# Kernel tuning notes

Hardware: AMD Instinct MI355X
Metric: run time of the kernel (lower is better)

The kernel has to match this reference:

```python
import jax, jax.numpy as jnp
import numpy as np

NBINS = 256


def _getmask(mi):
    # mi: [h, w] image already scaled to [0, 255]
    # torch.histc(mi, bins=256, min=0, max=255): values outside [0,255] ignored
    hist = jax.lax.stop_gradient(
        jnp.histogram(mi, bins=NBINS, range=(0.0, 255.0))[0].astype(jnp.float32)
    )
    # mask_output[i] = sum_j |j - i| * hist[j]  -> small 256x256 matvec
    j = jnp.arange(NBINS, dtype=jnp.float32)
    dist = jnp.abs(j[:, None] - j[None, :])  # [256, 256]
    mask_output = dist @ hist                 # [256]
    # mask[image==i] = mask_output[i]; only exact-integer pixels in [0,255] match
    r = jnp.round(mi)
    valid = (mi == r) & (r >= 0.0) & (r <= 255.0)
    idx = jnp.clip(r, 0.0, 255.0).astype(jnp.int32)
    mask = jnp.where(valid, mask_output[idx], 0.0)
    # if mask.max()==0: return zeros; else return the (scaled) image itself
    return jnp.where(mask.max() == 0.0, jnp.zeros_like(mi), mi)


def _forward(image_irr, image_vis):
    irr = image_irr * 255.0
    _vis = image_vis * 255.0  # computed but unused in the original forward
    mi = irr[:, 0, :, :]                       # [b, h, w]
    masked = jax.vmap(_getmask)(mi) / 255.0    # [b, h, w]
    msk_ir = masked[:, None, :, :]             # [b, 1, h, w]
    msk = jnp.stack([msk_ir, 1.0 - msk_ir], axis=0)  # [2, b, 1, h, w]
    msks = jax.nn.softmax(msk, axis=0)
    return msks[0], msks[1]


def setup_inputs() -> dict:
    key = jax.random.key(0)
    k1, k2 = jax.random.split(key)
    shape = (16, 1, 1024, 1024)
    # quantized pixels so that image*255 is (mostly) exactly integer,
    # matching the module's implicit assumption (histc + equality tests)
    image_irr = jax.random.randint(k1, shape, 0, 256).astype(jnp.float32) / 255.0
    image_vis = jax.random.randint(k2, shape, 0, 256).astype(jnp.float32) / 255.0
    return {"image_irr": image_irr, "image_vis": image_vis}


def reference(image_irr, image_vis):
    return _forward(image_irr, image_vis)
```

## Files before the change

### kernel.cpp

```cpp
#include <hip/hip_runtime.h>
#include <stdint.h>

#define BATCH 16
#define HW (1024*1024)
#define NPIX (BATCH * HW)
#define SBLK 64

typedef float vf4 __attribute__((ext_vector_type(4)));

__global__ __launch_bounds__(256) void scan_kernel(const float* __restrict__ in,
                                                   uint2* __restrict__ partials) {
    const int tid = threadIdx.x;
    const int batch = blockIdx.y;
    int minb = 0x7FFF, maxb = -1, valid = 0;

    const vf4* src = (const vf4*)(in + (size_t)batch * HW) + (size_t)blockIdx.x * 4096;
    for (int i = tid; i < 4096; i += 256) {
        vf4 x = __builtin_nontemporal_load(&src[i]);
        float v[4] = {x.x, x.y, x.z, x.w};
#pragma unroll
        for (int k = 0; k < 4; ++k) {
            float mi = v[k] * 255.0f;
            if (mi >= 0.0f && mi <= 255.0f) {
                int b = (int)(mi * (256.0f / 255.0f));
                if (b > 255) b = 255;
                minb = min(minb, b);
                maxb = max(maxb, b);
                valid |= (mi == rintf(mi)) ? 1 : 0;
            }
        }
    }
#pragma unroll
    for (int off = 32; off > 0; off >>= 1) {
        minb  = min(minb, __shfl_xor(minb, off));
        maxb  = max(maxb, __shfl_xor(maxb, off));
        valid |= __shfl_xor(valid, off);
    }
    __shared__ int sm[4], sx[4], sv[4];
    const int w = tid >> 6;
    if ((tid & 63) == 0) { sm[w] = minb; sx[w] = maxb; sv[w] = valid; }
    __syncthreads();
    if (tid == 0) {
#pragma unroll
        for (int i = 1; i < 4; ++i) {
            minb  = min(minb, sm[i]);
            maxb  = max(maxb, sx[i]);
            valid |= sv[i];
        }
        uint2 p;
        p.x = ((unsigned)(minb & 0xFFFF) << 16) | (unsigned)(maxb & 0xFFFF);
        p.y = (unsigned)valid;
        partials[batch * SBLK + blockIdx.x] = p;
    }
}

__global__ __launch_bounds__(64) void flag_kernel(const uint2* __restrict__ partials,
                                                  unsigned* __restrict__ flags) {
    const int b = blockIdx.x;
    const int t = threadIdx.x;
    uint2 p = partials[b * SBLK + t];
    int minb = (int)(short)(p.x >> 16);
    int maxb = (int)(short)(p.x & 0xFFFF);
    unsigned valid = p.y;
#pragma unroll
    for (int off = 32; off > 0; off >>= 1) {
        minb = min(minb, __shfl_xor(minb, off));
        maxb = max(maxb, __shfl_xor(maxb, off));
        valid |= (unsigned)__shfl_xor((int)valid, off);
    }
    if (t == 0) flags[b] = (valid && (minb != maxb)) ? 1u : 0u;
}

__device__ __forceinline__ float2 softmax2(float x, float fm) {
    float mi = x * 255.0f;
    float m = (mi / 255.0f) * fm;
    float e = expf(1.0f - 2.0f * m);
    float r = 1.0f / (1.0f + e);
    return make_float2(r, e * r);
}

__global__ __launch_bounds__(256) void out_kernel(const float* __restrict__ in,
                                                  const unsigned* __restrict__ flags,
                                                  float* __restrict__ out) {
    const int batch = blockIdx.x >> 10;
    const float fm = flags[batch] ? 1.0f : 0.0f;
    const size_t i4 = (size_t)blockIdx.x * 256 + threadIdx.x;
    vf4 x = __builtin_nontemporal_load(&((const vf4*)in)[i4]);
    float2 rx = softmax2(x.x, fm);
    float2 ry = softmax2(x.y, fm);
    float2 rz = softmax2(x.z, fm);
    float2 rw = softmax2(x.w, fm);
    vf4 o0 = {rx.x, ry.x, rz.x, rw.x};
    vf4 o1 = {rx.y, ry.y, rz.y, rw.y};
    __builtin_nontemporal_store(o0, &((vf4*)out)[i4]);
    __builtin_nontemporal_store(o1, &((vf4*)(out + (size_t)NPIX))[i4]);
}

extern "C" void kernel_launch(void* const* d_in, const int* in_sizes, int n_in,
                              void* d_out, int out_size, void* d_ws, size_t ws_size,
                              hipStream_t stream) {
    const float* irr = (const float*)d_in[0];
    float* out = (float*)d_out;

    uint2* partials = (uint2*)d_ws;
    unsigned* flags = (unsigned*)(partials + BATCH * SBLK);

    scan_kernel<<<dim3(SBLK, BATCH), 256, 0, stream>>>(irr, partials);
    flag_kernel<<<BATCH, 64, 0, stream>>>(partials, flags);
    out_kernel<<<NPIX / 4 / 256, 256, 0, stream>>>(irr, flags, out);
}
```

Baseline: 224.9 us.

## Fuse flag reduction into output kernel and process four vectors per thread

Removes the separate flag kernel launch: each output block now reduces its batch's 64 scan partials in one wavefront and shares the flag through shared memory. The output kernel handles four float4 vectors per thread with a quarter as many blocks. Input loads in both scan and output kernels switch from nontemporal to regular loads, so the second read of the input can hit in cache. The cost is that the partials reduction is repeated in every output block, plus a block barrier before any output is written.

```diff
diff --git a/kernel.cpp b/kernel.cpp
--- a/kernel.cpp
+++ b/kernel.cpp
@@ -16,7 +16,7 @@
 
     const vf4* src = (const vf4*)(in + (size_t)batch * HW) + (size_t)blockIdx.x * 4096;
     for (int i = tid; i < 4096; i += 256) {
-        vf4 x = __builtin_nontemporal_load(&src[i]);
+        vf4 x = src[i];
         float v[4] = {x.x, x.y, x.z, x.w};
 #pragma unroll
         for (int k = 0; k < 4; ++k) {
@@ -54,23 +54,6 @@
     }
 }
 
-__global__ __launch_bounds__(64) void flag_kernel(const uint2* __restrict__ partials,
-                                                  unsigned* __restrict__ flags) {
-    const int b = blockIdx.x;
-    const int t = threadIdx.x;
-    uint2 p = partials[b * SBLK + t];
-    int minb = (int)(short)(p.x >> 16);
-    int maxb = (int)(short)(p.x & 0xFFFF);
-    unsigned valid = p.y;
-#pragma unroll
-    for (int off = 32; off > 0; off >>= 1) {
-        minb = min(minb, __shfl_xor(minb, off));
-        maxb = max(maxb, __shfl_xor(maxb, off));
-        valid |= (unsigned)__shfl_xor((int)valid, off);
-    }
-    if (t == 0) flags[b] = (valid && (minb != maxb)) ? 1u : 0u;
-}
-
 __device__ __forceinline__ float2 softmax2(float x, float fm) {
     float mi = x * 255.0f;
     float m = (mi / 255.0f) * fm;
@@ -80,20 +63,43 @@
 }
 
 __global__ __launch_bounds__(256) void out_kernel(const float* __restrict__ in,
-                                                  const unsigned* __restrict__ flags,
+                                                  const uint2* __restrict__ partials,
                                                   float* __restrict__ out) {
-    const int batch = blockIdx.x >> 10;
-    const float fm = flags[batch] ? 1.0f : 0.0f;
-    const size_t i4 = (size_t)blockIdx.x * 256 + threadIdx.x;
-    vf4 x = __builtin_nontemporal_load(&((const vf4*)in)[i4]);
-    float2 rx = softmax2(x.x, fm);
-    float2 ry = softmax2(x.y, fm);
-    float2 rz = softmax2(x.z, fm);
-    float2 rw = softmax2(x.w, fm);
-    vf4 o0 = {rx.x, ry.x, rz.x, rw.x};
-    vf4 o1 = {rx.y, ry.y, rz.y, rw.y};
-    __builtin_nontemporal_store(o0, &((vf4*)out)[i4]);
-    __builtin_nontemporal_store(o1, &((vf4*)(out + (size_t)NPIX))[i4]);
+    const int batch = blockIdx.x >> 8;
+    __shared__ float sflag;
+    if (threadIdx.x < 64) {
+        uint2 p = partials[batch * SBLK + threadIdx.x];
+        int minb = (int)(short)(p.x >> 16);
+        int maxb = (int)(short)(p.x & 0xFFFF);
+        unsigned valid = p.y;
+#pragma unroll
+        for (int off = 32; off > 0; off >>= 1) {
+            minb = min(minb, __shfl_xor(minb, off));
+            maxb = max(maxb, __shfl_xor(maxb, off));
+            valid |= (unsigned)__shfl_xor((int)valid, off);
+        }
+        if (threadIdx.x == 0) sflag = (valid && (minb != maxb)) ? 1.0f : 0.0f;
+    }
+    __syncthreads();
+    const float fm = sflag;
+
+    const size_t base = (size_t)blockIdx.x * 1024 + threadIdx.x;
+    const vf4* pin = (const vf4*)in;
+    vf4* pout0 = (vf4*)out;
+    vf4* pout1 = (vf4*)(out + (size_t)NPIX);
+#pragma unroll
+    for (int j = 0; j < 4; ++j) {
+        const size_t i4 = base + j * 256;
+        vf4 x = pin[i4];
+        float2 rx = softmax2(x.x, fm);
+        float2 ry = softmax2(x.y, fm);
+        float2 rz = softmax2(x.z, fm);
+        float2 rw = softmax2(x.w, fm);
+        vf4 o0 = {rx.x, ry.x, rz.x, rw.x};
+        vf4 o1 = {rx.y, ry.y, rz.y, rw.y};
+        __builtin_nontemporal_store(o0, &pout0[i4]);
+        __builtin_nontemporal_store(o1, &pout1[i4]);
+    }
 }
 
 extern "C" void kernel_launch(void* const* d_in, const int* in_sizes, int n_in,
@@ -103,9 +109,7 @@
     float* out = (float*)d_out;
 
     uint2* partials = (uint2*)d_ws;
-    unsigned* flags = (unsigned*)(partials + BATCH * SBLK);
 
     scan_kernel<<<dim3(SBLK, BATCH), 256, 0, stream>>>(irr, partials);
-    flag_kernel<<<BATCH, 64, 0, stream>>>(partials, flags);
-    out_kernel<<<NPIX / 4 / 256, 256, 0, stream>>>(irr, flags, out);
+    out_kernel<<<NPIX / 16 / 256, 256, 0, stream>>>(irr, partials, out);
 }
```

Measured after the change: 226.0 us. Within noise of the previous version (+0.5%).
